# Optimization experiments

Measured on AMD Instinct MI355X. Metric: run time of the kernel, lower is better.

## Reference

```python
import jax, jax.numpy as jnp
import numpy as np

HIDDEN = 768
NUM_HEADS = 12
HEAD_DIM = HIDDEN // NUM_HEADS
QMAX = 127.0
DOMAIN_MIN, DOMAIN_MAX = -10.0, 0.0
NUM_INTERVALS = 12


def _build_pla_coeffs():
    # Least-squares linear fit of exp(x) on each of 12 uniform intervals of [-10, 0].
    xs = np.linspace(DOMAIN_MIN, DOMAIN_MAX, 1001)
    ys = np.exp(xs)
    edges = np.linspace(DOMAIN_MIN, DOMAIN_MAX, NUM_INTERVALS + 1)
    ms, cs = [], []
    for i in range(NUM_INTERVALS):
        mask = (xs >= edges[i]) & (xs <= edges[i + 1])
        m, c = np.polyfit(xs[mask], ys[mask], 1)
        ms.append(m)
        cs.append(c)
    # 'intervals' buffer holds the left endpoints a_i (length 12), as in torch code
    return (np.asarray(ms, np.float32), np.asarray(cs, np.float32),
            edges[:NUM_INTERVALS].astype(np.float32))

_PLA_M, _PLA_C, _PLA_A = _build_pla_coeffs()


def pla_exp(x):
    m = jnp.asarray(_PLA_M)
    c = jnp.asarray(_PLA_C)
    a = jnp.asarray(_PLA_A)
    xc = jnp.clip(x, DOMAIN_MIN, DOMAIN_MAX)
    # sum(xc >= a_i) - 1 == searchsorted(a, xc, side='right') - 1 (a is sorted)
    idx = jnp.clip(jnp.searchsorted(a, xc, side='right') - 1, 0, NUM_INTERVALS - 2)
    return m[idx] * xc + c[idx]


def pla_softmax(scores):
    shifted = scores - jnp.max(scores, axis=-1, keepdims=True)
    exps = pla_exp(shifted)
    return exps / (jnp.sum(exps, axis=-1, keepdims=True) + 1e-9)


def quant_linear(x, w_int8, w_scale, bias):
    # Dynamic per-token symmetric int8 quantization of activations.
    abs_max = jnp.max(jnp.abs(x), axis=-1, keepdims=True)
    input_scale = abs_max / QMAX
    input_scale = jnp.where(input_scale == 0.0, 1.0, input_scale)
    x_q = jnp.clip(jnp.round(x / input_scale), -128.0, 127.0)  # int8 values in fp32
    out = x_q @ w_int8.astype(jnp.float32).T                   # simulated int32 accum
    out = out * w_scale * input_scale                          # dequant rescale
    return out + bias


def setup_inputs() -> dict:
    key = jax.random.key(0)
    ks = jax.random.split(key, 16)
    B, S = 4, 1024
    inp = {
        'hidden_states': jax.random.normal(ks[0], (B, S, HIDDEN), jnp.float32),
        'attention_mask': jnp.zeros((B, 1, 1, S), jnp.float32),
    }
    for i, name in enumerate(['q', 'k', 'v', 'o']):
        kw, ksc, kb = ks[1 + 3 * i], ks[2 + 3 * i], ks[3 + 3 * i]
        inp[f'w{name}_int8'] = jax.random.randint(kw, (HIDDEN, HIDDEN), 0, 256, jnp.int32) - 128
        inp[f'w{name}_scale'] = jax.random.uniform(ksc, (HIDDEN,), jnp.float32) * 1e-4
        inp[f'b{name}'] = jax.random.normal(kb, (HIDDEN,), jnp.float32)
    return inp


def reference(hidden_states, attention_mask,
              wq_int8, wq_scale, bq,
              wk_int8, wk_scale, bk,
              wv_int8, wv_scale, bv,
              wo_int8, wo_scale, bo):
    B, S, H = hidden_states.shape
    scale = HEAD_DIM ** -0.5

    def split_heads(x):  # [B,S,H] -> [B,nh,S,hd]
        return x.reshape(B, S, NUM_HEADS, HEAD_DIM).transpose(0, 2, 1, 3)

    q = split_heads(quant_linear(hidden_states, wq_int8, wq_scale, bq))
    k = split_heads(quant_linear(hidden_states, wk_int8, wk_scale, bk))
    v = split_heads(quant_linear(hidden_states, wv_int8, wv_scale, bv))

    attn_scores = jnp.einsum('bhqd,bhkd->bhqk', q, k) * scale
    attn_scores = attn_scores + attention_mask
    attn_probs = pla_softmax(attn_scores)  # dropout is identity in eval mode

    context = jnp.einsum('bhqk,bhkd->bhqd', attn_probs, v)
    context = context.transpose(0, 2, 1, 3).reshape(B, S, H)
    return quant_linear(context, wo_int8, wo_scale, bo)
```

## Files before the change

### kernel.cpp

```cpp
#include <hip/hip_runtime.h>
#include <stdint.h>
#include <cmath>

#define TOKENS 4096
#define HIDDEN 768
#define NHEADS 12
#define SEQ    1024
#define NBH    48

typedef int   int32x4 __attribute__((ext_vector_type(4)));
typedef float f32x4   __attribute__((ext_vector_type(4)));
typedef short short8  __attribute__((ext_vector_type(8)));

struct PlaCoeffs { float m[12]; float c[12]; };

#define WBYTES   ((size_t)HIDDEN * HIDDEN)
#define OFF_WQ    ((size_t)256)
#define OFF_WK    (OFF_WQ + WBYTES)
#define OFF_WV    (OFF_WK + WBYTES)
#define OFF_WO    (OFF_WV + WBYTES)
#define OFF_XQ1   (OFF_WO + WBYTES)
#define OFF_SC1   (OFF_XQ1 + (size_t)TOKENS * HIDDEN)
#define OFF_QH    (OFF_SC1 + (size_t)TOKENS * 4)
#define HB        ((size_t)NBH * SEQ * 64 * 2)
#define OFF_KH    (OFF_QH + HB)
#define OFF_VT    (OFF_KH + HB)
#define OFF_CTX   (OFF_VT + HB)
#define OFF_XQ2   (OFF_CTX + (size_t)TOKENS * HIDDEN * 4)
#define OFF_SC2   (OFF_XQ2 + (size_t)TOKENS * HIDDEN)

__device__ __forceinline__ unsigned short f2bf(float f) {
  unsigned int u = __float_as_uint(f);
  u = (u + 0x7fffu + ((u >> 16) & 1u)) >> 16;
  return (unsigned short)u;
}

static PlaCoeffs compute_pla_coeffs() {
  PlaCoeffs out;
  const double step_e = 10.0 / 12.0;
  for (int i = 0; i < 12; i++) {
    double e0 = (double)i * step_e + (-10.0);
    double e1 = (i + 1 == 12) ? 0.0 : (double)(i + 1) * step_e + (-10.0);
    double n = 0.0, Sx = 0.0, Sy = 0.0, Sxy = 0.0, Sxx = 0.0;
    for (int j = 0; j <= 1000; j++) {
      double x = (j == 1000) ? 0.0 : (double)j * 0.01 + (-10.0);
      if (x >= e0 && x <= e1) {
        double y = std::exp(x);
        n += 1.0; Sx += x; Sy += y; Sxy += x * y; Sxx += x * x;
      }
    }
    double det = n * Sxx - Sx * Sx;
    double m = (n * Sxy - Sx * Sy) / det;
    double c = (Sy - m * Sx) / n;
    out.m[i] = (float)m;
    out.c[i] = (float)c;
  }
  return out;
}
static const PlaCoeffs g_pla = compute_pla_coeffs();

__global__ void pack_w(const int* __restrict__ w0, const int* __restrict__ w1,
                       const int* __restrict__ w2, const int* __restrict__ w3,
                       signed char* __restrict__ o0, signed char* __restrict__ o1,
                       signed char* __restrict__ o2, signed char* __restrict__ o3) {
  int z = blockIdx.y;
  const int* src = z == 0 ? w0 : z == 1 ? w1 : z == 2 ? w2 : w3;
  signed char* dst = z == 0 ? o0 : z == 1 ? o1 : z == 2 ? o2 : o3;
  int idx = (blockIdx.x * 256 + threadIdx.x) * 4;
  int32x4 v = *(const int32x4*)(src + idx);
  int packed = (v[0] & 255) | ((v[1] & 255) << 8) | ((v[2] & 255) << 16) | (v[3] << 24);
  *(int*)(dst + idx) = packed;
}

__global__ void quant_kernel(const float* __restrict__ x, signed char* __restrict__ xq,
                             float* __restrict__ sc) {
  int t = blockIdx.x;
  int tid = threadIdx.x;
  const float* row = x + (size_t)t * HIDDEN;
  float v0 = row[tid], v1 = row[tid + 256], v2 = row[tid + 512];
  float am = fmaxf(fabsf(v0), fmaxf(fabsf(v1), fabsf(v2)));
#pragma unroll
  for (int m = 1; m < 64; m <<= 1) am = fmaxf(am, __shfl_xor(am, m, 64));
  __shared__ float red[4];
  if ((tid & 63) == 0) red[tid >> 6] = am;
  __syncthreads();
  float total = fmaxf(fmaxf(red[0], red[1]), fmaxf(red[2], red[3]));
  float s = total / 127.0f;
  if (s == 0.0f) s = 1.0f;
  float q0 = fminf(fmaxf(rintf(v0 / s), -128.0f), 127.0f);
  float q1 = fminf(fmaxf(rintf(v1 / s), -128.0f), 127.0f);
  float q2 = fminf(fmaxf(rintf(v2 / s), -128.0f), 127.0f);
  signed char* orow = xq + (size_t)t * HIDDEN;
  orow[tid]       = (signed char)(int)q0;
  orow[tid + 256] = (signed char)(int)q1;
  orow[tid + 512] = (signed char)(int)q2;
  if (tid == 0) sc[t] = s;
}

__device__ __forceinline__ void i8_mainloop(const signed char* __restrict__ Abase,
                                            const signed char* __restrict__ Bbase,
                                            char* As, char* Bs, int tid,
                                            int32x4 acc[4][4]) {
  int lane = tid & 63, w = tid >> 6;
  int lr = lane & 15, lg = lane >> 4;
  int wr = w >> 1, wc = w & 1;
  int laneoff = (lane >> 3) * HIDDEN + (((lane & 7) ^ (lane >> 3)) * 16);
  int rowblk = w * 32;

#pragma unroll
  for (int ii = 0; ii < 4; ii++) {
    const signed char* sa = Abase + (size_t)(rowblk + ii * 8) * HIDDEN + laneoff;
    const signed char* sb = Bbase + (size_t)(rowblk + ii * 8) * HIDDEN + laneoff;
    __builtin_amdgcn_global_load_lds(
        (const __attribute__((address_space(1))) void*)sa,
        (__attribute__((address_space(3))) void*)(As + (w * 4 + ii) * 1024), 16, 0, 0);
    __builtin_amdgcn_global_load_lds(
        (const __attribute__((address_space(1))) void*)sb,
        (__attribute__((address_space(3))) void*)(Bs + (w * 4 + ii) * 1024), 16, 0, 0);
  }
  __syncthreads();

  int buf = 0;
  for (int ks = 0; ks < 6; ks++) {
    if (ks < 5) {
      char* An = As + (buf ^ 1) * 16384;
      char* Bn = Bs + (buf ^ 1) * 16384;
#pragma unroll
      for (int ii = 0; ii < 4; ii++) {
        const signed char* sa =
            Abase + (size_t)(rowblk + ii * 8) * HIDDEN + (ks + 1) * 128 + laneoff;
        const signed char* sb =
            Bbase + (size_t)(rowblk + ii * 8) * HIDDEN + (ks + 1) * 128 + laneoff;
        __builtin_amdgcn_global_load_lds(
            (const __attribute__((address_space(1))) void*)sa,
            (__attribute__((address_space(3))) void*)(An + (w * 4 + ii) * 1024), 16, 0, 0);
        __builtin_amdgcn_global_load_lds(
            (const __attribute__((address_space(1))) void*)sb,
            (__attribute__((address_space(3))) void*)(Bn + (w * 4 + ii) * 1024), 16, 0, 0);
      }
    }
    const char* Ac = As + buf * 16384;
    const char* Bc = Bs + buf * 16384;
#pragma unroll
    for (int ksub = 0; ksub < 2; ksub++) {
      int32x4 af[4], bf[4];
      int cs = (ksub * 4 + lg) ^ (lr & 7);
#pragma unroll
      for (int i = 0; i < 4; i++)
        af[i] = *(const int32x4*)(Ac + (wr * 64 + i * 16 + lr) * 128 + cs * 16);
#pragma unroll
      for (int j = 0; j < 4; j++)
        bf[j] = *(const int32x4*)(Bc + (wc * 64 + j * 16 + lr) * 128 + cs * 16);
#pragma unroll
      for (int i = 0; i < 4; i++)
#pragma unroll
        for (int j = 0; j < 4; j++)
          acc[i][j] = __builtin_amdgcn_mfma_i32_16x16x64_i8(af[i], bf[j], acc[i][j], 0, 0, 0);
    }
    __syncthreads();
    buf ^= 1;
  }
}

__launch_bounds__(256, 2)
__global__ void qkv_gemm(const signed char* __restrict__ xq, const float* __restrict__ isc,
                         const signed char* __restrict__ wq, const signed char* __restrict__ wk,
                         const signed char* __restrict__ wv,
                         const float* __restrict__ wsq, const float* __restrict__ wsk,
                         const float* __restrict__ wsv,
                         const float* __restrict__ bq, const float* __restrict__ bk,
                         const float* __restrict__ bv,
                         unsigned short* __restrict__ qh, unsigned short* __restrict__ kh,
                         unsigned short* __restrict__ vt) {
  __shared__ __align__(16) char As[2 * 16384];
  __shared__ __align__(16) char Bs[2 * 16384];
  int z = blockIdx.z;
  const signed char* w   = z == 0 ? wq  : z == 1 ? wk  : wv;
  const float*       wsc = z == 0 ? wsq : z == 1 ? wsk : wsv;
  const float*       bias= z == 0 ? bq  : z == 1 ? bk  : bv;
  unsigned short*    out = z == 0 ? qh  : z == 1 ? kh  : vt;

  int tid = threadIdx.x;
  int lane = tid & 63, wave = tid >> 6;
  int lr = lane & 15, lg = lane >> 4;
  int mbase = blockIdx.x * 128 + (wave >> 1) * 64;
  int nbase = blockIdx.y * 128 + (wave & 1) * 64;

  int32x4 acc[4][4];
#pragma unroll
  for (int i = 0; i < 4; i++)
#pragma unroll
    for (int j = 0; j < 4; j++) acc[i][j] = (int32x4){0, 0, 0, 0};

  i8_mainloop(xq + (size_t)blockIdx.x * 128 * HIDDEN,
              w + (size_t)blockIdx.y * 128 * HIDDEN, As, Bs, tid, acc);

#pragma unroll
  for (int j = 0; j < 4; j++) {
    int col = nbase + j * 16 + lr;
    float wsv_ = wsc[col], bv_ = bias[col];
    int h = col >> 6, d = col & 63;
#pragma unroll
    for (int i = 0; i < 4; i++) {
#pragma unroll
      for (int r = 0; r < 4; r++) {
        int trow = mbase + i * 16 + lg * 4 + r;
        float v = (float)acc[i][j][r] * wsv_ * isc[trow] + bv_;
        int bb = trow >> 10, ss = trow & 1023;
        size_t off;
        if (z < 2) off = (((size_t)(bb * NHEADS + h)) * SEQ + ss) * 64 + d;
        else       off = (((size_t)(bb * NHEADS + h)) * 64 + d) * SEQ + ss;
        out[off] = f2bf(v);
      }
    }
  }
}

__launch_bounds__(256, 2)
__global__ void o_gemm(const signed char* __restrict__ xq, const float* __restrict__ isc,
                       const signed char* __restrict__ w, const float* __restrict__ wsc,
                       const float* __restrict__ bias, float* __restrict__ out) {
  __shared__ __align__(16) char As[2 * 16384];
  __shared__ __align__(16) char Bs[2 * 16384];
  int tid = threadIdx.x;
  int lane = tid & 63, wave = tid >> 6;
  int lr = lane & 15, lg = lane >> 4;
  int mbase = blockIdx.x * 128 + (wave >> 1) * 64;
  int nbase = blockIdx.y * 128 + (wave & 1) * 64;

  int32x4 acc[4][4];
#pragma unroll
  for (int i = 0; i < 4; i++)
#pragma unroll
    for (int j = 0; j < 4; j++) acc[i][j] = (int32x4){0, 0, 0, 0};

  i8_mainloop(xq + (size_t)blockIdx.x * 128 * HIDDEN,
              w + (size_t)blockIdx.y * 128 * HIDDEN, As, Bs, tid, acc);

#pragma unroll
  for (int j = 0; j < 4; j++) {
    int col = nbase + j * 16 + lr;
    float wsv_ = wsc[col], bv_ = bias[col];
#pragma unroll
    for (int i = 0; i < 4; i++) {
#pragma unroll
      for (int r = 0; r < 4; r++) {
        int trow = mbase + i * 16 + lg * 4 + r;
        float v = (float)acc[i][j][r] * wsv_ * isc[trow] + bv_;
        out[(size_t)trow * HIDDEN + col] = v;
      }
    }
  }
}

__launch_bounds__(512, 6)
__global__ void attn_kernel(const unsigned short* __restrict__ qh,
                            const unsigned short* __restrict__ kgl,
                            const unsigned short* __restrict__ vt,
                            const float* __restrict__ mask,
                            const PlaCoeffs cf,
                            float* __restrict__ ctx) {
  __shared__ __align__(16) char smem[49152];
  unsigned short* kbuf = (unsigned short*)smem;
  unsigned short* vbuf = (unsigned short*)(smem + 16384);
  unsigned short* plds = (unsigned short*)(smem + 32768);
  float* parts = (float*)smem;
  __shared__ float rmaxp[8][16], rmaxv[4][16], rsump[8][16], rsumv[4][16];
  __shared__ float2 lmc[12];

  int tid = threadIdx.x;
  int lane = tid & 63, w = tid >> 6;
  int lr = lane & 15, lg = lane >> 4;
  int m = w & 3, kh2 = w >> 2;

  if (tid < 12) lmc[tid] = make_float2(cf.m[tid], cf.c[tid]);

  int nb = (blockIdx.x & 7) * 96 + (blockIdx.x >> 3);
  int bh = nb >> 4, qt = nb & 15;
  int b = bh / NHEADS, h = bh % NHEADS;
  int qbase = qt * 64;

  const unsigned short* qp     = qh + ((size_t)bh * SEQ + qbase + m * 16) * 64;
  const unsigned short* khead  = kgl + (size_t)bh * SEQ * 64;
  const unsigned short* vthead = vt + (size_t)bh * 64 * SEQ;
  const float* mrow = mask + b * SEQ;

  short8 qa0 = *(const short8*)(qp + (size_t)lr * 64 + lg * 8);
  short8 qa1 = *(const short8*)(qp + (size_t)lr * 64 + 32 + lg * 8);

  int sr = tid >> 3, sd = (tid & 7) * 8;
  int sidx = sr * 64 + (sd ^ ((sr & 7) << 3));
  const unsigned short* kgp = khead + (size_t)sr * 64 + sd;
  const unsigned short* vgp = vthead + (size_t)sr * 1024 + sd;

  float rm[4] = {-3.0e38f, -3.0e38f, -3.0e38f, -3.0e38f};
  short8 stk = *(const short8*)kgp;
  for (int c = 0; c < 16; c++) {
    unsigned short* kb = kbuf + (c & 1) * 4096;
    *(short8*)(kb + sidx) = stk;
    if (c < 15) stk = *(const short8*)(kgp + (size_t)(c + 1) * 4096);
    __syncthreads();
#pragma unroll
    for (int kt = 0; kt < 2; kt++) {
      int krow = kh2 * 32 + kt * 16 + lr;
      const unsigned short* kbp = kb + krow * 64;
      int sw = (krow & 7) << 3;
      short8 k0 = *(const short8*)(kbp + ((lg * 8) ^ sw));
      short8 k1 = *(const short8*)(kbp + ((32 + lg * 8) ^ sw));
      f32x4 a = {0.f, 0.f, 0.f, 0.f};
      __builtin_amdgcn_s_setprio(1);
      a = __builtin_amdgcn_mfma_f32_16x16x32_bf16(qa0, k0, a, 0, 0, 0);
      a = __builtin_amdgcn_mfma_f32_16x16x32_bf16(qa1, k1, a, 0, 0, 0);
      __builtin_amdgcn_s_setprio(0);
      float mk = mrow[c * 64 + krow];
#pragma unroll
      for (int r = 0; r < 4; r++) rm[r] = fmaxf(rm[r], fmaf(a[r], 0.125f, mk));
    }
  }
#pragma unroll
  for (int r = 0; r < 4; r++) {
#pragma unroll
    for (int msk = 1; msk < 16; msk <<= 1) rm[r] = fmaxf(rm[r], __shfl_xor(rm[r], msk, 64));
  }
  if (lr == 0) {
#pragma unroll
    for (int r = 0; r < 4; r++) rmaxp[w][lg * 4 + r] = rm[r];
  }
  __syncthreads();
  if (tid < 64) {
    int mm = tid >> 4, row = tid & 15;
    rmaxv[mm][row] = fmaxf(rmaxp[mm][row], rmaxp[mm + 4][row]);
  }
  __syncthreads();

  float rmx[4], rs[4];
#pragma unroll
  for (int r = 0; r < 4; r++) { rmx[r] = rmaxv[m][lg * 4 + r]; rs[r] = 0.f; }
  f32x4 pacc[4];
#pragma unroll
  for (int n = 0; n < 4; n++) pacc[n] = (f32x4){0.f, 0.f, 0.f, 0.f};
  unsigned short* pw = plds + w * 1024;

  short8 stk2 = *(const short8*)kgp;
  short8 stv  = *(const short8*)vgp;
  for (int c = 0; c < 16; c++) {
    unsigned short* kb = kbuf + (c & 1) * 4096;
    unsigned short* vb = vbuf + (c & 1) * 4096;
    *(short8*)(kb + sidx) = stk2;
    *(short8*)(vb + sidx) = stv;
    if (c < 15) {
      stk2 = *(const short8*)(kgp + (size_t)(c + 1) * 4096);
      stv  = *(const short8*)(vgp + (c + 1) * 64);
    }
    __syncthreads();
#pragma unroll
    for (int kt = 0; kt < 2; kt++) {
      int krow = kh2 * 32 + kt * 16 + lr;
      const unsigned short* kbp = kb + krow * 64;
      int sw = (krow & 7) << 3;
      short8 k0 = *(const short8*)(kbp + ((lg * 8) ^ sw));
      short8 k1 = *(const short8*)(kbp + ((32 + lg * 8) ^ sw));
      f32x4 a = {0.f, 0.f, 0.f, 0.f};
      __builtin_amdgcn_s_setprio(1);
      a = __builtin_amdgcn_mfma_f32_16x16x32_bf16(qa0, k0, a, 0, 0, 0);
      a = __builtin_amdgcn_mfma_f32_16x16x32_bf16(qa1, k1, a, 0, 0, 0);
      __builtin_amdgcn_s_setprio(0);
      float mk = mrow[c * 64 + krow];
#pragma unroll
      for (int r = 0; r < 4; r++) {
        int row = lg * 4 + r;
        float x = fmaf(a[r], 0.125f, mk) - rmx[r];
        x = fminf(fmaxf(x, -10.f), 0.f);
        int ii = (int)((x + 10.f) * 1.2f);
        ii = ii > 10 ? 10 : ii;
        float2 mc = lmc[ii];
        float p = mc.x * x + mc.y;
        rs[r] += p;
        pw[row * 64 + ((kt * 16 + lr) ^ ((row & 7) << 3))] = f2bf(p);
      }
    }
    short8 pa = *(const short8*)(pw + lr * 64 + ((lg * 8) ^ ((lr & 7) << 3)));
    __builtin_amdgcn_s_setprio(1);
#pragma unroll
    for (int n = 0; n < 4; n++) {
      int d = n * 16 + lr;
      short8 vv = *(const short8*)(vb + d * 64 + ((kh2 * 32 + lg * 8) ^ ((d & 7) << 3)));
      pacc[n] = __builtin_amdgcn_mfma_f32_16x16x32_bf16(pa, vv, pacc[n], 0, 0, 0);
    }
    __builtin_amdgcn_s_setprio(0);
  }

#pragma unroll
  for (int r = 0; r < 4; r++) {
#pragma unroll
    for (int msk = 1; msk < 16; msk <<= 1) rs[r] += __shfl_xor(rs[r], msk, 64);
  }
  if (lr == 0) {
#pragma unroll
    for (int r = 0; r < 4; r++) rsump[w][lg * 4 + r] = rs[r];
  }
  __syncthreads();
  {
    float* pslice = parts + w * 1024;
#pragma unroll
    for (int n = 0; n < 4; n++)
#pragma unroll
      for (int r = 0; r < 4; r++)
        pslice[(lg * 4 + r) * 64 + n * 16 + lr] = pacc[n][r];
  }
  if (tid < 64) {
    int mm = tid >> 4, row = tid & 15;
    rsumv[mm][row] = rsump[mm][row] + rsump[mm + 4][row];
  }
  __syncthreads();

  {
    int mm = tid >> 7, row = (tid >> 3) & 15, c8 = (tid & 7) * 8;
    float dn = rsumv[mm][row] + 1e-9f;
    const float* p0 = parts + (mm * 16 + row) * 64 + c8;
    const float* p1 = p0 + 4 * 1024;
    f32x4 a0 = *(const f32x4*)p0, a1 = *(const f32x4*)(p0 + 4);
    f32x4 b0 = *(const f32x4*)p1, b1 = *(const f32x4*)(p1 + 4);
    f32x4 o0 = {(a0[0] + b0[0]) / dn, (a0[1] + b0[1]) / dn,
                (a0[2] + b0[2]) / dn, (a0[3] + b0[3]) / dn};
    f32x4 o1 = {(a1[0] + b1[0]) / dn, (a1[1] + b1[1]) / dn,
                (a1[2] + b1[2]) / dn, (a1[3] + b1[3]) / dn};
    float* op = &ctx[((size_t)b * SEQ + qbase + mm * 16 + row) * HIDDEN + h * 64 + c8];
    *(f32x4*)op = o0;
    *(f32x4*)(op + 4) = o1;
  }
}

extern "C" void kernel_launch(void* const* d_in, const int* in_sizes, int n_in,
                              void* d_out, int out_size, void* d_ws, size_t ws_size,
                              hipStream_t stream) {
  const float* hidden = (const float*)d_in[0];
  const float* mask   = (const float*)d_in[1];
  const int*   wq  = (const int*)d_in[2];
  const float* wsq = (const float*)d_in[3];
  const float* bq  = (const float*)d_in[4];
  const int*   wk  = (const int*)d_in[5];
  const float* wsk = (const float*)d_in[6];
  const float* bk  = (const float*)d_in[7];
  const int*   wv  = (const int*)d_in[8];
  const float* wsv = (const float*)d_in[9];
  const float* bv  = (const float*)d_in[10];
  const int*   wo  = (const int*)d_in[11];
  const float* wso = (const float*)d_in[12];
  const float* bo  = (const float*)d_in[13];

  char* ws = (char*)d_ws;
  signed char*    pwq   = (signed char*)(ws + OFF_WQ);
  signed char*    pwk   = (signed char*)(ws + OFF_WK);
  signed char*    pwv   = (signed char*)(ws + OFF_WV);
  signed char*    pwo   = (signed char*)(ws + OFF_WO);
  signed char*    xq1   = (signed char*)(ws + OFF_XQ1);
  float*          sc1   = (float*)(ws + OFF_SC1);
  unsigned short* qhp   = (unsigned short*)(ws + OFF_QH);
  unsigned short* khp   = (unsigned short*)(ws + OFF_KH);
  unsigned short* vtp   = (unsigned short*)(ws + OFF_VT);
  float*          ctxp  = (float*)(ws + OFF_CTX);
  signed char*    xq2   = (signed char*)(ws + OFF_XQ2);
  float*          sc2   = (float*)(ws + OFF_SC2);

  pack_w<<<dim3(576, 4), 256, 0, stream>>>(wq, wk, wv, wo, pwq, pwk, pwv, pwo);
  quant_kernel<<<TOKENS, 256, 0, stream>>>(hidden, xq1, sc1);
  qkv_gemm<<<dim3(32, 6, 3), 256, 0, stream>>>(xq1, sc1, pwq, pwk, pwv,
                                               wsq, wsk, wsv, bq, bk, bv,
                                               qhp, khp, vtp);
  attn_kernel<<<768, 512, 0, stream>>>(qhp, khp, vtp, mask, g_pla, ctxp);
  quant_kernel<<<TOKENS, 256, 0, stream>>>(ctxp, xq2, sc2);
  o_gemm<<<dim3(32, 6, 1), 256, 0, stream>>>(xq2, sc2, pwo, wso, bo, (float*)d_out);
}
```

Measured before the change: 101.8 us.

## Fuse weight packing with input quant, stage V-transpose via LDS, pack bf16 converts

Weight packing and first-layer activation quantization are merged into one launch so that one kernel launch and its tail are removed. The V projection epilogue now writes bf16 values into an LDS tile with an XOR swizzle, then stores the transposed layout with coalesced 16-byte global writes. Before, each 2-byte scattered store had a stride of SEQ. The attention softmax now uses the hardware packed bf16 convert and fmaf-based interval indexing. The convert uses round-to-nearest in hardware rather than the manual rounding routine, which could change low bits slightly.

```diff
diff --git a/kernel.cpp b/kernel.cpp
--- a/kernel.cpp
+++ b/kernel.cpp
@@ -35,6 +35,12 @@
   return (unsigned short)u;
 }
 
+__device__ __forceinline__ unsigned int cvtpk_bf16(float a, float b) {
+  unsigned int r;
+  asm volatile("v_cvt_pk_bf16_f32 %0, %1, %2" : "=v"(r) : "v"(a), "v"(b));
+  return r;
+}
+
 static PlaCoeffs compute_pla_coeffs() {
   PlaCoeffs out;
   const double step_e = 10.0 / 12.0;
@@ -59,17 +65,44 @@
 }
 static const PlaCoeffs g_pla = compute_pla_coeffs();
 
-__global__ void pack_w(const int* __restrict__ w0, const int* __restrict__ w1,
-                       const int* __restrict__ w2, const int* __restrict__ w3,
-                       signed char* __restrict__ o0, signed char* __restrict__ o1,
-                       signed char* __restrict__ o2, signed char* __restrict__ o3) {
-  int z = blockIdx.y;
-  const int* src = z == 0 ? w0 : z == 1 ? w1 : z == 2 ? w2 : w3;
-  signed char* dst = z == 0 ? o0 : z == 1 ? o1 : z == 2 ? o2 : o3;
-  int idx = (blockIdx.x * 256 + threadIdx.x) * 4;
-  int32x4 v = *(const int32x4*)(src + idx);
-  int packed = (v[0] & 255) | ((v[1] & 255) << 8) | ((v[2] & 255) << 16) | (v[3] << 24);
-  *(int*)(dst + idx) = packed;
+__global__ void prep_kernel(const float* __restrict__ x, signed char* __restrict__ xq,
+                            float* __restrict__ sc,
+                            const int* __restrict__ w0, const int* __restrict__ w1,
+                            const int* __restrict__ w2, const int* __restrict__ w3,
+                            signed char* __restrict__ o0, signed char* __restrict__ o1,
+                            signed char* __restrict__ o2, signed char* __restrict__ o3) {
+  int tid = threadIdx.x;
+  if (blockIdx.x < TOKENS) {
+    int t = blockIdx.x;
+    const float* row = x + (size_t)t * HIDDEN;
+    float v0 = row[tid], v1 = row[tid + 256], v2 = row[tid + 512];
+    float am = fmaxf(fabsf(v0), fmaxf(fabsf(v1), fabsf(v2)));
+#pragma unroll
+    for (int m = 1; m < 64; m <<= 1) am = fmaxf(am, __shfl_xor(am, m, 64));
+    __shared__ float red[4];
+    if ((tid & 63) == 0) red[tid >> 6] = am;
+    __syncthreads();
+    float total = fmaxf(fmaxf(red[0], red[1]), fmaxf(red[2], red[3]));
+    float s = total / 127.0f;
+    if (s == 0.0f) s = 1.0f;
+    float q0 = fminf(fmaxf(rintf(v0 / s), -128.0f), 127.0f);
+    float q1 = fminf(fmaxf(rintf(v1 / s), -128.0f), 127.0f);
+    float q2 = fminf(fmaxf(rintf(v2 / s), -128.0f), 127.0f);
+    signed char* orow = xq + (size_t)t * HIDDEN;
+    orow[tid]       = (signed char)(int)q0;
+    orow[tid + 256] = (signed char)(int)q1;
+    orow[tid + 512] = (signed char)(int)q2;
+    if (tid == 0) sc[t] = s;
+  } else {
+    int p = blockIdx.x - TOKENS;
+    int z = p / 576, px = p % 576;
+    const int* src = z == 0 ? w0 : z == 1 ? w1 : z == 2 ? w2 : w3;
+    signed char* dst = z == 0 ? o0 : z == 1 ? o1 : z == 2 ? o2 : o3;
+    int idx = (px * 256 + tid) * 4;
+    int32x4 v = *(const int32x4*)(src + idx);
+    int packed = (v[0] & 255) | ((v[1] & 255) << 8) | ((v[2] & 255) << 16) | (v[3] << 24);
+    *(int*)(dst + idx) = packed;
+  }
 }
 
 __global__ void quant_kernel(const float* __restrict__ x, signed char* __restrict__ xq,
@@ -183,7 +216,8 @@
   int tid = threadIdx.x;
   int lane = tid & 63, wave = tid >> 6;
   int lr = lane & 15, lg = lane >> 4;
-  int mbase = blockIdx.x * 128 + (wave >> 1) * 64;
+  int mbase0 = blockIdx.x * 128;
+  int mbase = mbase0 + (wave >> 1) * 64;
   int nbase = blockIdx.y * 128 + (wave & 1) * 64;
 
   int32x4 acc[4][4];
@@ -192,26 +226,57 @@
 #pragma unroll
     for (int j = 0; j < 4; j++) acc[i][j] = (int32x4){0, 0, 0, 0};
 
-  i8_mainloop(xq + (size_t)blockIdx.x * 128 * HIDDEN,
+  i8_mainloop(xq + (size_t)mbase0 * HIDDEN,
               w + (size_t)blockIdx.y * 128 * HIDDEN, As, Bs, tid, acc);
 
-#pragma unroll
-  for (int j = 0; j < 4; j++) {
-    int col = nbase + j * 16 + lr;
-    float wsv_ = wsc[col], bv_ = bias[col];
-    int h = col >> 6, d = col & 63;
-#pragma unroll
-    for (int i = 0; i < 4; i++) {
-#pragma unroll
-      for (int r = 0; r < 4; r++) {
-        int trow = mbase + i * 16 + lg * 4 + r;
-        float v = (float)acc[i][j][r] * wsv_ * isc[trow] + bv_;
-        int bb = trow >> 10, ss = trow & 1023;
-        size_t off;
-        if (z < 2) off = (((size_t)(bb * NHEADS + h)) * SEQ + ss) * 64 + d;
-        else       off = (((size_t)(bb * NHEADS + h)) * 64 + d) * SEQ + ss;
-        out[off] = f2bf(v);
+  if (z < 2) {
+#pragma unroll
+    for (int j = 0; j < 4; j++) {
+      int col = nbase + j * 16 + lr;
+      float wsv_ = wsc[col], bv_ = bias[col];
+      int h = col >> 6, d = col & 63;
+#pragma unroll
+      for (int i = 0; i < 4; i++) {
+#pragma unroll
+        for (int r = 0; r < 4; r++) {
+          int trow = mbase + i * 16 + lg * 4 + r;
+          float v = (float)acc[i][j][r] * wsv_ * isc[trow] + bv_;
+          int bb = trow >> 10, ss = trow & 1023;
+          out[(((size_t)(bb * NHEADS + h)) * SEQ + ss) * 64 + d] = f2bf(v);
+        }
       }
+    }
+  } else {
+    unsigned short* T = (unsigned short*)As;
+#pragma unroll
+    for (int j = 0; j < 4; j++) {
+      int colc = (wave & 1) * 64 + j * 16 + lr;
+      int gcol = blockIdx.y * 128 + colc;
+      float wsv_ = wsc[gcol], bv_ = bias[gcol];
+      int rlb = (wave >> 1) * 64 + lg * 4;
+#pragma unroll
+      for (int i = 0; i < 4; i++) {
+        int rl = rlb + i * 16;
+        float v0 = (float)acc[i][j][0] * wsv_ * isc[mbase0 + rl + 0] + bv_;
+        float v1 = (float)acc[i][j][1] * wsv_ * isc[mbase0 + rl + 1] + bv_;
+        float v2 = (float)acc[i][j][2] * wsv_ * isc[mbase0 + rl + 2] + bv_;
+        float v3 = (float)acc[i][j][3] * wsv_ * isc[mbase0 + rl + 3] + bv_;
+        int oct = (rl >> 3) ^ (colc & 7);
+        unsigned short* dst = T + colc * 128 + (oct << 3) + (rl & 7);
+        *(unsigned int*)(dst)     = cvtpk_bf16(v0, v1);
+        *(unsigned int*)(dst + 2) = cvtpk_bf16(v2, v3);
+      }
+    }
+    __syncthreads();
+    int bb = mbase0 >> 10, ssb = mbase0 & 1023;
+    int o = tid & 15, cb = (tid >> 4) * 8;
+#pragma unroll
+    for (int j = 0; j < 8; j++) {
+      int colc = cb + j;
+      int gcol = blockIdx.y * 128 + colc;
+      int hh = gcol >> 6, dd = gcol & 63;
+      unsigned short* g = out + (((size_t)(bb * NHEADS + hh)) * 64 + dd) * SEQ + ssb + o * 8;
+      *(short8*)g = *(const short8*)(T + colc * 128 + ((o ^ (colc & 7)) << 3));
     }
   }
 }
@@ -366,18 +431,25 @@
       a = __builtin_amdgcn_mfma_f32_16x16x32_bf16(qa1, k1, a, 0, 0, 0);
       __builtin_amdgcn_s_setprio(0);
       float mk = mrow[c * 64 + krow];
+      float p[4];
 #pragma unroll
       for (int r = 0; r < 4; r++) {
-        int row = lg * 4 + r;
         float x = fmaf(a[r], 0.125f, mk) - rmx[r];
         x = fminf(fmaxf(x, -10.f), 0.f);
-        int ii = (int)((x + 10.f) * 1.2f);
+        int ii = (int)fmaf(x, 1.2f, 12.0f);
         ii = ii > 10 ? 10 : ii;
         float2 mc = lmc[ii];
-        float p = mc.x * x + mc.y;
-        rs[r] += p;
-        pw[row * 64 + ((kt * 16 + lr) ^ ((row & 7) << 3))] = f2bf(p);
+        p[r] = fmaf(mc.x, x, mc.y);
+        rs[r] += p[r];
       }
+      unsigned int pk01 = cvtpk_bf16(p[0], p[1]);
+      unsigned int pk23 = cvtpk_bf16(p[2], p[3]);
+      int colw = kt * 16 + lr;
+      int r0 = lg * 4;
+      pw[(r0 + 0) * 64 + (colw ^ (((r0 + 0) & 7) << 3))] = (unsigned short)pk01;
+      pw[(r0 + 1) * 64 + (colw ^ (((r0 + 1) & 7) << 3))] = (unsigned short)(pk01 >> 16);
+      pw[(r0 + 2) * 64 + (colw ^ (((r0 + 2) & 7) << 3))] = (unsigned short)pk23;
+      pw[(r0 + 3) * 64 + (colw ^ (((r0 + 3) & 7) << 3))] = (unsigned short)(pk23 >> 16);
     }
     short8 pa = *(const short8*)(pw + lr * 64 + ((lg * 8) ^ ((lr & 7) << 3)));
     __builtin_amdgcn_s_setprio(1);
@@ -463,8 +535,8 @@
   signed char*    xq2   = (signed char*)(ws + OFF_XQ2);
   float*          sc2   = (float*)(ws + OFF_SC2);
 
-  pack_w<<<dim3(576, 4), 256, 0, stream>>>(wq, wk, wv, wo, pwq, pwk, pwv, pwo);
-  quant_kernel<<<TOKENS, 256, 0, stream>>>(hidden, xq1, sc1);
+  prep_kernel<<<TOKENS + 2304, 256, 0, stream>>>(hidden, xq1, sc1,
+                                                 wq, wk, wv, wo, pwq, pwk, pwv, pwo);
   qkv_gemm<<<dim3(32, 6, 3), 256, 0, stream>>>(xq1, sc1, pwq, pwk, pwv,
                                                wsq, wsk, wsv, bq, bk, bv,
                                                qhp, khp, vtp);
```

Result: faster. 93.19 us, median of 3 (-8.5%).
